# Optimization experiments

Measured on AMD Instinct MI355X. Metric: run time of the kernel, lower is better.

## Reference

```python
import jax, jax.numpy as jnp
import numpy as np

B, IN, NC, O, H = 256, 2048, 1000, 4096, 4  # batch, in_features, num_classes, n_decoders, hidden
NEG_SLOPE = 0.1

def setup_inputs() -> dict:
    key = jax.random.key(0)
    ks = jax.random.split(key, 7)
    s1 = 1.0 / np.sqrt(IN)
    s2 = 1.0 / np.sqrt(H)
    return {
        "x":   jax.random.normal(ks[0], (B, IN), jnp.float32),
        "fcW": jax.random.normal(ks[1], (NC, IN), jnp.float32) * s1,
        "fcb": jax.random.normal(ks[2], (NC,), jnp.float32) * s1,
        "W1":  jax.random.normal(ks[3], (O, IN, H), jnp.float32) * s1,
        "b1":  jax.random.normal(ks[4], (O, H), jnp.float32) * s1,
        "W2":  jax.random.normal(ks[5], (O, H), jnp.float32) * s2,
        "b2":  jax.random.normal(ks[6], (O,), jnp.float32) * s2,
    }

def reference(x, fcW, fcb, W1, b1, W2, b2):
    # fc head: x1 = x @ fcW^T + fcb  -> [B, NC]
    x1 = jnp.einsum("bi,ci->bc", x, fcW) + fcb
    # 4096 tiny MLPs batched into one grouped GEMM:
    # h = leaky_relu(x @ W1_o + b1_o) for each decoder o  -> [B, O, H]
    h = jnp.einsum("bi,oih->boh", x, W1) + b1
    h = jnp.where(h >= 0, h, NEG_SLOPE * h)
    # second layer (H->1) collapses to a weighted reduction -> [B, O]
    x2 = jnp.einsum("boh,oh->bo", h, W2) + b2
    return (x1, x2)
```

## Files before the change

### kernel.cpp

```cpp
#include <hip/hip_runtime.h>


typedef __bf16 bf16_t;
typedef __bf16 bf16x8 __attribute__((ext_vector_type(8)));
typedef __bf16 bf16x4 __attribute__((ext_vector_type(4)));
typedef float  f32x4  __attribute__((ext_vector_type(4)));

#define LDS_STRIDE 40

__global__ __launch_bounds__(256, 2)
void fused_dual(const float* __restrict__ x,
                const float* __restrict__ fcW,
                const float* __restrict__ fcb,
                const float* __restrict__ W1,
                const float* __restrict__ b1,
                const float* __restrict__ W2,
                const float* __restrict__ b2,
                float* __restrict__ out)
{
    __shared__ bf16_t lA[256 * LDS_STRIDE];
    __shared__ bf16_t lB[64  * LDS_STRIDE];

    const int tid   = threadIdx.x;
    const int blk   = blockIdx.x;
    const bool is_fc = (blk < 16);
    const int c0    = (is_fc ? blk : (blk - 16)) * 64;

    const int a_col4 = tid & 7;
    const int a_r0   = tid >> 3;
    const int b_n    = tid >> 2;
    const int b_kb   = tid & 3;

    const float* ap = x + a_r0 * 2048 + a_col4 * 4;
    const float* bp;
    if (is_fc) {
        int row = c0 + b_n; if (row > 999) row = 999;
        bp = fcW + row * 2048 + b_kb * 8;
    } else {
        const int o = (c0 >> 2) + (b_n >> 2);
        bp = W1 + o * 8192 + b_kb * 32 + (b_n & 3);
    }

    float4 aR[8];
    float  bR[8];

    #pragma unroll
    for (int r = 0; r < 8; ++r) aR[r] = *(const float4*)(ap + r * (32 * 2048));
    if (is_fc) {
        float4 t0 = *(const float4*)bp;
        float4 t1 = *(const float4*)(bp + 4);
        bR[0] = t0.x; bR[1] = t0.y; bR[2] = t0.z; bR[3] = t0.w;
        bR[4] = t1.x; bR[5] = t1.y; bR[6] = t1.z; bR[7] = t1.w;
    } else {
        #pragma unroll
        for (int j = 0; j < 8; ++j) bR[j] = bp[j * 4];
    }

    const int wav  = tid >> 6;
    const int lane = tid & 63;
    const int l15  = lane & 15;
    const int quad = lane >> 4;

    f32x4 acc[4][4];
    #pragma unroll
    for (int i = 0; i < 4; ++i)
        #pragma unroll
        for (int j = 0; j < 4; ++j) acc[i][j] = (f32x4){0.f, 0.f, 0.f, 0.f};

    char* lAb = (char*)lA;
    char* lBb = (char*)lB;
    const int aWbase = a_r0 * (LDS_STRIDE * 2) + a_col4 * 8;
    const int bWbase = b_n  * (LDS_STRIDE * 2) + b_kb * 16;

    for (int kt = 0; kt < 64; ++kt) {
        __syncthreads();
        #pragma unroll
        for (int r = 0; r < 8; ++r) {
            bf16x4 v;
            v[0] = (bf16_t)aR[r].x; v[1] = (bf16_t)aR[r].y;
            v[2] = (bf16_t)aR[r].z; v[3] = (bf16_t)aR[r].w;
            *(bf16x4*)(lAb + aWbase + r * (32 * LDS_STRIDE * 2)) = v;
        }
        {
            bf16x8 v;
            #pragma unroll
            for (int j = 0; j < 8; ++j) v[j] = (bf16_t)bR[j];
            *(bf16x8*)(lBb + bWbase) = v;
        }
        __syncthreads();
        if (kt != 63) {
            ap += 32;
            bp += is_fc ? 32 : 128;
            #pragma unroll
            for (int r = 0; r < 8; ++r) aR[r] = *(const float4*)(ap + r * (32 * 2048));
            if (is_fc) {
                float4 t0 = *(const float4*)bp;
                float4 t1 = *(const float4*)(bp + 4);
                bR[0] = t0.x; bR[1] = t0.y; bR[2] = t0.z; bR[3] = t0.w;
                bR[4] = t1.x; bR[5] = t1.y; bR[6] = t1.z; bR[7] = t1.w;
            } else {
                #pragma unroll
                for (int j = 0; j < 8; ++j) bR[j] = bp[j * 4];
            }
        }
        bf16x8 af[4], bfr[4];
        #pragma unroll
        for (int mt = 0; mt < 4; ++mt)
            af[mt] = *(const bf16x8*)(lAb + (wav * 64 + mt * 16 + l15) * (LDS_STRIDE * 2) + quad * 16);
        #pragma unroll
        for (int nt = 0; nt < 4; ++nt)
            bfr[nt] = *(const bf16x8*)(lBb + (nt * 16 + l15) * (LDS_STRIDE * 2) + quad * 16);
        #pragma unroll
        for (int mt = 0; mt < 4; ++mt)
            #pragma unroll
            for (int nt = 0; nt < 4; ++nt)
                acc[mt][nt] = __builtin_amdgcn_mfma_f32_16x16x32_bf16(af[mt], bfr[nt], acc[mt][nt], 0, 0, 0);
    }

    if (is_fc) {
        #pragma unroll
        for (int nt = 0; nt < 4; ++nt) {
            const int c = c0 + nt * 16 + l15;
            const bool valid = (c < 1000);
            const float bias = valid ? fcb[c] : 0.f;
            #pragma unroll
            for (int mt = 0; mt < 4; ++mt) {
                #pragma unroll
                for (int r = 0; r < 4; ++r) {
                    if (valid) {
                        const int row = wav * 64 + mt * 16 + quad * 4 + r;
                        out[row * 1000 + c] = acc[mt][nt][r] + bias;
                    }
                }
            }
        }
    } else {
        float* x2out = out + 256 * 1000;
        #pragma unroll
        for (int nt = 0; nt < 4; ++nt) {
            const int c   = c0 + nt * 16 + l15;
            const float b1v = b1[c];
            const float w2v = W2[c];
            const int o   = c >> 2;
            const float b2v = b2[o];
            #pragma unroll
            for (int mt = 0; mt < 4; ++mt) {
                #pragma unroll
                for (int r = 0; r < 4; ++r) {
                    float h = acc[mt][nt][r] + b1v;
                    h = (h >= 0.f) ? h : 0.1f * h;
                    float wv = h * w2v;
                    wv += __shfl_xor(wv, 1, 64);
                    wv += __shfl_xor(wv, 2, 64);
                    if ((lane & 3) == 0) {
                        const int row = wav * 64 + mt * 16 + quad * 4 + r;
                        x2out[row * 4096 + o] = wv + b2v;
                    }
                }
            }
        }
    }
}

extern "C" void kernel_launch(void* const* d_in, const int* in_sizes, int n_in,
                              void* d_out, int out_size, void* d_ws, size_t ws_size,
                              hipStream_t stream)
{
    (void)in_sizes; (void)n_in; (void)d_ws; (void)ws_size; (void)out_size;
    const float* x   = (const float*)d_in[0];
    const float* fcW = (const float*)d_in[1];
    const float* fcb = (const float*)d_in[2];
    const float* W1  = (const float*)d_in[3];
    const float* b1  = (const float*)d_in[4];
    const float* W2  = (const float*)d_in[5];
    const float* b2  = (const float*)d_in[6];
    fused_dual<<<272, 256, 0, stream>>>(x, fcW, fcb, W1, b1, W2, b2, (float*)d_out);
}
```

Before: 270.5 us.

## Split batch rows across four blocks to raise grid size and occupancy

Each block now computes a 64x64 output tile instead of 256x64, so the grid grows fourfold and more blocks fit per CU (launch bounds raised to 4). The K tile per iteration doubles to 64 with a wider LDS stride, halving loop trips and barriers. The aim is to hide the latency of streaming the large W1 weight tensor with more concurrent work. In exchange, each weight tile is loaded by four blocks, relying on L2 sharing between adjacent blocks, and per-block MFMA reuse drops.

After: 293.6 us. 1.09x slower.

```diff
diff --git a/kernel.cpp b/kernel.cpp
--- a/kernel.cpp
+++ b/kernel.cpp
@@ -6,9 +6,9 @@
 typedef __bf16 bf16x4 __attribute__((ext_vector_type(4)));
 typedef float  f32x4  __attribute__((ext_vector_type(4)));
 
-#define LDS_STRIDE 40
+#define LDSTR 72
 
-__global__ __launch_bounds__(256, 2)
+__global__ __launch_bounds__(256, 4)
 void fused_dual(const float* __restrict__ x,
                 const float* __restrict__ fcW,
                 const float* __restrict__ fcb,
@@ -18,42 +18,46 @@
                 const float* __restrict__ b2,
                 float* __restrict__ out)
 {
-    __shared__ bf16_t lA[256 * LDS_STRIDE];
-    __shared__ bf16_t lB[64  * LDS_STRIDE];
+    __shared__ bf16_t lA[64 * LDSTR];
+    __shared__ bf16_t lB[64 * LDSTR];
 
-    const int tid   = threadIdx.x;
-    const int blk   = blockIdx.x;
-    const bool is_fc = (blk < 16);
-    const int c0    = (is_fc ? blk : (blk - 16)) * 64;
+    const int tid = threadIdx.x;
+    const int blk = blockIdx.x;
+    const int cg  = blk >> 2;
+    const int rg  = blk & 3;
+    const int m0  = rg * 64;
+    const bool is_fc = (cg < 16);
+    const int c0  = (is_fc ? cg : cg - 16) * 64;
 
-    const int a_col4 = tid & 7;
-    const int a_r0   = tid >> 3;
-    const int b_n    = tid >> 2;
-    const int b_kb   = tid & 3;
+    const int a_row = tid >> 4;
+    const int a_c4  = tid & 15;
+    const int b_n  = tid >> 2;
+    const int b_kb = tid & 3;
 
-    const float* ap = x + a_r0 * 2048 + a_col4 * 4;
+    const float* ap = x + (m0 + a_row) * 2048 + a_c4 * 4;
     const float* bp;
     if (is_fc) {
         int row = c0 + b_n; if (row > 999) row = 999;
-        bp = fcW + row * 2048 + b_kb * 8;
+        bp = fcW + row * 2048 + b_kb * 16;
     } else {
         const int o = (c0 >> 2) + (b_n >> 2);
-        bp = W1 + o * 8192 + b_kb * 32 + (b_n & 3);
+        bp = W1 + o * 8192 + b_kb * 64 + (b_n & 3);
     }
 
-    float4 aR[8];
-    float  bR[8];
+    float4 aR[4];
+    float  bR[16];
 
     #pragma unroll
-    for (int r = 0; r < 8; ++r) aR[r] = *(const float4*)(ap + r * (32 * 2048));
+    for (int r = 0; r < 4; ++r) aR[r] = *(const float4*)(ap + r * (16 * 2048));
     if (is_fc) {
-        float4 t0 = *(const float4*)bp;
-        float4 t1 = *(const float4*)(bp + 4);
-        bR[0] = t0.x; bR[1] = t0.y; bR[2] = t0.z; bR[3] = t0.w;
-        bR[4] = t1.x; bR[5] = t1.y; bR[6] = t1.z; bR[7] = t1.w;
+        #pragma unroll
+        for (int q = 0; q < 4; ++q) {
+            float4 t = *(const float4*)(bp + q * 4);
+            bR[q*4+0] = t.x; bR[q*4+1] = t.y; bR[q*4+2] = t.z; bR[q*4+3] = t.w;
+        }
     } else {
         #pragma unroll
-        for (int j = 0; j < 8; ++j) bR[j] = bp[j * 4];
+        for (int j = 0; j < 16; ++j) bR[j] = bp[j * 4];
     }
 
     const int wav  = tid >> 6;
@@ -61,60 +65,57 @@
     const int l15  = lane & 15;
     const int quad = lane >> 4;
 
-    f32x4 acc[4][4];
+    f32x4 acc[4];
     #pragma unroll
-    for (int i = 0; i < 4; ++i)
-        #pragma unroll
-        for (int j = 0; j < 4; ++j) acc[i][j] = (f32x4){0.f, 0.f, 0.f, 0.f};
+    for (int nt = 0; nt < 4; ++nt) acc[nt] = (f32x4){0.f, 0.f, 0.f, 0.f};
 
     char* lAb = (char*)lA;
     char* lBb = (char*)lB;
-    const int aWbase = a_r0 * (LDS_STRIDE * 2) + a_col4 * 8;
-    const int bWbase = b_n  * (LDS_STRIDE * 2) + b_kb * 16;
+    const int aW = (a_row) * (LDSTR * 2) + a_c4 * 8;
+    const int bW = b_n * (LDSTR * 2) + b_kb * 32;
 
-    for (int kt = 0; kt < 64; ++kt) {
+    for (int kt = 0; kt < 32; ++kt) {
         __syncthreads();
         #pragma unroll
-        for (int r = 0; r < 8; ++r) {
+        for (int r = 0; r < 4; ++r) {
             bf16x4 v;
             v[0] = (bf16_t)aR[r].x; v[1] = (bf16_t)aR[r].y;
             v[2] = (bf16_t)aR[r].z; v[3] = (bf16_t)aR[r].w;
-            *(bf16x4*)(lAb + aWbase + r * (32 * LDS_STRIDE * 2)) = v;
+            *(bf16x4*)(lAb + aW + r * (16 * LDSTR * 2)) = v;
         }
         {
-            bf16x8 v;
+            bf16x8 v0, v1;
             #pragma unroll
-            for (int j = 0; j < 8; ++j) v[j] = (bf16_t)bR[j];
-            *(bf16x8*)(lBb + bWbase) = v;
+            for (int j = 0; j < 8; ++j) { v0[j] = (bf16_t)bR[j]; v1[j] = (bf16_t)bR[8 + j]; }
+            *(bf16x8*)(lBb + bW)      = v0;
+            *(bf16x8*)(lBb + bW + 16) = v1;
         }
         __syncthreads();
-        if (kt != 63) {
-            ap += 32;
-            bp += is_fc ? 32 : 128;
+        if (kt != 31) {
+            ap += 64;
+            bp += is_fc ? 64 : 256;
             #pragma unroll
-            for (int r = 0; r < 8; ++r) aR[r] = *(const float4*)(ap + r * (32 * 2048));
+            for (int r = 0; r < 4; ++r) aR[r] = *(const float4*)(ap + r * (16 * 2048));
             if (is_fc) {
-                float4 t0 = *(const float4*)bp;
-                float4 t1 = *(const float4*)(bp + 4);
-                bR[0] = t0.x; bR[1] = t0.y; bR[2] = t0.z; bR[3] = t0.w;
-                bR[4] = t1.x; bR[5] = t1.y; bR[6] = t1.z; bR[7] = t1.w;
+                #pragma unroll
+                for (int q = 0; q < 4; ++q) {
+                    float4 t = *(const float4*)(bp + q * 4);
+                    bR[q*4+0] = t.x; bR[q*4+1] = t.y; bR[q*4+2] = t.z; bR[q*4+3] = t.w;
+                }
             } else {
                 #pragma unroll
-                for (int j = 0; j < 8; ++j) bR[j] = bp[j * 4];
+                for (int j = 0; j < 16; ++j) bR[j] = bp[j * 4];
             }
         }
-        bf16x8 af[4], bfr[4];
         #pragma unroll
-        for (int mt = 0; mt < 4; ++mt)
-            af[mt] = *(const bf16x8*)(lAb + (wav * 64 + mt * 16 + l15) * (LDS_STRIDE * 2) + quad * 16);
-        #pragma unroll
-        for (int nt = 0; nt < 4; ++nt)
-            bfr[nt] = *(const bf16x8*)(lBb + (nt * 16 + l15) * (LDS_STRIDE * 2) + quad * 16);
-        #pragma unroll
-        for (int mt = 0; mt < 4; ++mt)
+        for (int kk = 0; kk < 2; ++kk) {
+            bf16x8 af = *(const bf16x8*)(lAb + (wav * 16 + l15) * (LDSTR * 2) + kk * 64 + quad * 16);
             #pragma unroll
-            for (int nt = 0; nt < 4; ++nt)
-                acc[mt][nt] = __builtin_amdgcn_mfma_f32_16x16x32_bf16(af[mt], bfr[nt], acc[mt][nt], 0, 0, 0);
+            for (int nt = 0; nt < 4; ++nt) {
+                bf16x8 bf = *(const bf16x8*)(lBb + (nt * 16 + l15) * (LDSTR * 2) + kk * 64 + quad * 16);
+                acc[nt] = __builtin_amdgcn_mfma_f32_16x16x32_bf16(af, bf, acc[nt], 0, 0, 0);
+            }
+        }
     }
 
     if (is_fc) {
@@ -122,15 +123,12 @@
         for (int nt = 0; nt < 4; ++nt) {
             const int c = c0 + nt * 16 + l15;
             const bool valid = (c < 1000);
-            const float bias = valid ? fcb[c] : 0.f;
+            const float bias = fcb[valid ? c : 999];
             #pragma unroll
-            for (int mt = 0; mt < 4; ++mt) {
-                #pragma unroll
-                for (int r = 0; r < 4; ++r) {
-                    if (valid) {
-                        const int row = wav * 64 + mt * 16 + quad * 4 + r;
-                        out[row * 1000 + c] = acc[mt][nt][r] + bias;
-                    }
+            for (int r = 0; r < 4; ++r) {
+                if (valid) {
+                    const int row = m0 + wav * 16 + quad * 4 + r;
+                    out[row * 1000 + c] = acc[nt][r] + bias;
                 }
             }
         }
@@ -144,18 +142,15 @@
             const int o   = c >> 2;
             const float b2v = b2[o];
             #pragma unroll
-            for (int mt = 0; mt < 4; ++mt) {
-                #pragma unroll
-                for (int r = 0; r < 4; ++r) {
-                    float h = acc[mt][nt][r] + b1v;
-                    h = (h >= 0.f) ? h : 0.1f * h;
-                    float wv = h * w2v;
-                    wv += __shfl_xor(wv, 1, 64);
-                    wv += __shfl_xor(wv, 2, 64);
-                    if ((lane & 3) == 0) {
-                        const int row = wav * 64 + mt * 16 + quad * 4 + r;
-                        x2out[row * 4096 + o] = wv + b2v;
-                    }
+            for (int r = 0; r < 4; ++r) {
+                float h = acc[nt][r] + b1v;
+                h = (h >= 0.f) ? h : 0.1f * h;
+                float wv = h * w2v;
+                wv += __shfl_xor(wv, 1, 64);
+                wv += __shfl_xor(wv, 2, 64);
+                if ((lane & 3) == 0) {
+                    const int row = m0 + wav * 16 + quad * 4 + r;
+                    x2out[row * 4096 + o] = wv + b2v;
                 }
             }
         }
@@ -174,5 +169,5 @@
     const float* b1  = (const float*)d_in[4];
     const float* W2  = (const float*)d_in[5];
     const float* b2  = (const float*)d_in[6];
-    fused_dual<<<272, 256, 0, stream>>>(x, fcW, fcb, W1, b1, W2, b2, (float*)d_out);
+    fused_dual<<<1088, 256, 0, stream>>>(x, fcW, fcb, W1, b1, W2, b2, (float*)d_out);
 }
```
